# Optimization experiments

Hardware: AMD Instinct MI355X
Metric: run time of the kernel (lower is better)

Reference implementation:

```python
import jax, jax.numpy as jnp
import numpy as np

B = 65536
NE = 256   # n_encode
NH = 256   # n_hidden
NC = 4     # n_command
D = 64     # n_depth (BatchNorm channels)
F = 32     # n_features
M = D * (F // 2)  # 1024
EPS = 1e-5


def setup_inputs() -> dict:
    key = jax.random.key(0)
    ks = jax.random.split(key, 8)
    s = 0.05
    return {
        "feature": jax.random.normal(ks[0], (B, NE), jnp.float32),
        "hidden":  jax.random.normal(ks[1], (B, NH), jnp.float32),
        "command": jax.random.normal(ks[2], (B, NC), jnp.float32),
        # linear weights (torch Linear stores [out, in]); xavier-like scale
        "Wq":  jax.random.normal(ks[3], (D, NC), jnp.float32) * s,
        "Wkz": jax.random.normal(ks[4], (M, NE), jnp.float32) * s,
        "Wkh": jax.random.normal(ks[5], (M, NH), jnp.float32) * s,
        "Wvz": jax.random.normal(ks[6], (M, NE), jnp.float32) * s,
        "Wvh": jax.random.normal(ks[7], (M, NH), jnp.float32) * s,
        # BatchNorm1d(64) affine params (normV exists in __init__ but is unused)
        "gammaQ": jnp.ones((D,), jnp.float32),
        "betaQ":  jnp.zeros((D,), jnp.float32),
        "gammaK": jnp.ones((D,), jnp.float32),
        "betaK":  jnp.zeros((D,), jnp.float32),
    }


def reference(feature, hidden, command, Wq, Wkz, Wkh, Wvz, Wvh,
              gammaQ, betaQ, gammaK, betaK):
    # Q projection: [B, D]; BatchNorm1d over batch (training-mode batch stats,
    # biased variance, matching torch).
    Q = command @ Wq.T
    mQ = jnp.mean(Q, axis=0)
    vQ = jnp.mean(jnp.square(Q - mQ), axis=0)
    Qn = (Q - mQ) / jnp.sqrt(vQ + EPS) * gammaQ + betaQ          # [B, D]

    # K: cat([B,M],[B,M]) -> [B, 2M] -> view [B, F, D] -> transpose -> [B, D, F]
    K = jnp.concatenate([feature @ Wkz.T, hidden @ Wkh.T], axis=1)
    K = K.reshape(-1, F, D).transpose(0, 2, 1)                    # [B, D, F]
    mK = jnp.mean(K, axis=(0, 2), keepdims=True)
    vK = jnp.mean(jnp.square(K - mK), axis=(0, 2), keepdims=True)
    Kn = (K - mK) / jnp.sqrt(vK + EPS) * gammaK[None, :, None] + betaK[None, :, None]

    # V: [B, F, D], NOT batch-normed (normV is dead code in the original)
    V = jnp.concatenate([feature @ Wvz.T, hidden @ Wvh.T], axis=1).reshape(-1, F, D)

    # attention: [B,1,D] @ [B,D,F] -> [B,F] scores; softmax over F; then @ V
    A = jax.nn.softmax(jnp.einsum('bd,bdf->bf', Qn, Kn) / np.sqrt(D).astype(np.float32), axis=-1)
    s = jnp.einsum('bf,bfd->bd', A, V)                            # [B, D]
    return s
```

## Files before the change

### kernel.cpp

```cpp
#include <hip/hip_runtime.h>
#include <hip/hip_bf16.h>
#include <math.h>


typedef float  f32x4   __attribute__((ext_vector_type(4)));
typedef float  f32x16  __attribute__((ext_vector_type(16)));
typedef __bf16 bf16x4  __attribute__((ext_vector_type(4)));
typedef __bf16 bf16x8  __attribute__((ext_vector_type(8)));

#define MFMA16(A, B, C) __builtin_amdgcn_mfma_f32_16x16x32_bf16((A), (B), (C), 0, 0, 0)
#define MFMA32(A, B, C) __builtin_amdgcn_mfma_f32_32x32x16_bf16((A), (B), (C), 0, 0, 0)

#define EPSV 1e-5f

#define WS_WV    0x000000u
#define WS_WKF   0x100000u
#define WS_G     0x120000u
#define WS_CS    0x1A0000u
#define WS_CMDP  0x1A0800u
#define WS_T     0x1A1800u
#define WS_U     0x1A3800u
#define WS_WQ2   0x1A5800u
#define WS_C0    0x1A5C00u

__global__ __launch_bounds__(512, 2) void setup1(const float* __restrict__ feat,
        const float* __restrict__ hid, const float4* __restrict__ cmd,
        const float* __restrict__ Wvz, const float* __restrict__ Wvh,
        __bf16* __restrict__ WV, float* __restrict__ CMDP, float* __restrict__ CS,
        __bf16* __restrict__ Gp)
{
    __shared__ __bf16 T[256 * 40];
    __shared__ float sm[8][14];
    const int blk = blockIdx.x;
    const int tid = threadIdx.x;

    if (blk >= 384) {
        const int b2 = blk - 384;
        float v[14];
#pragma unroll
        for (int k = 0; k < 14; ++k) v[k] = 0.f;
#pragma unroll
        for (int i = 0; i < 4; ++i) {
            float4 c = cmd[(b2 * 4 + i) * 512 + tid];
            v[0] += c.x;  v[1] += c.y;  v[2] += c.z;  v[3] += c.w;
            v[4] += c.x*c.x; v[5] += c.x*c.y; v[6] += c.x*c.z; v[7] += c.x*c.w;
            v[8] += c.y*c.y; v[9] += c.y*c.z; v[10] += c.y*c.w;
            v[11] += c.z*c.z; v[12] += c.z*c.w; v[13] += c.w*c.w;
        }
#pragma unroll
        for (int k = 0; k < 14; ++k) {
            float s = v[k];
#pragma unroll
            for (int off = 32; off; off >>= 1) s += __shfl_xor(s, off);
            if ((tid & 63) == 0) sm[tid >> 6][k] = s;
        }
        __syncthreads();
        if (tid < 14) {
            float s = 0.f;
#pragma unroll
            for (int w = 0; w < 8; ++w) s += sm[w][tid];
            CMDP[b2 * 14 + tid] = s;
        }
        return;
    }
    if (blk >= 128) {
        int t = (blk - 128) * 512 + tid;
        int e = t * 4;
        const float* src = (e < 262144) ? (Wvz + e) : (Wvh + (e - 262144));
        float4 a = *(const float4*)src;
        bf16x4 vv = { (__bf16)a.x, (__bf16)a.y, (__bf16)a.z, (__bf16)a.w };
        *(bf16x4*)(WV + e) = vv;
        return;
    }

    const int mat  = blk >> 6;
    const int chunk = blk & 63;
    const float* X = mat ? hid : feat;
    float* cs = CS + mat * 256;
    const int k0   = chunk * 1024;
    const int wid  = tid >> 6, lane = tid & 63, quad = lane >> 4, l15 = lane & 15;
    const int c    = tid & 255;
    const int t8   = tid >> 8;

    f32x4 acc[2][16];
#pragma unroll
    for (int mt = 0; mt < 2; ++mt)
#pragma unroll
        for (int nt = 0; nt < 16; ++nt) acc[mt][nt] = (f32x4){0.f, 0.f, 0.f, 0.f};

    float clsum = 0.f;
    for (int it = 0; it < 32; ++it) {
        __syncthreads();
        const int kb = k0 + it * 32;
#pragma unroll
        for (int i = 0; i < 16; ++i) {
            int k = t8 + 2 * i;
            float x = X[(size_t)(kb + k) * 256 + c];
            clsum += x;
            T[c * 40 + k] = (__bf16)x;
        }
        __syncthreads();
        bf16x8 a0 = *(const bf16x8*)&T[(wid * 32 +      l15) * 40 + quad * 8];
        bf16x8 a1 = *(const bf16x8*)&T[(wid * 32 + 16 + l15) * 40 + quad * 8];
#pragma unroll
        for (int nt = 0; nt < 16; ++nt) {
            bf16x8 b = *(const bf16x8*)&T[(nt * 16 + l15) * 40 + quad * 8];
            acc[0][nt] = MFMA16(a0, b, acc[0][nt]);
            acc[1][nt] = MFMA16(a1, b, acc[1][nt]);
        }
    }
    atomicAdd(&cs[c], clsum);
    __bf16* outp = Gp + (size_t)blk * 65536;
#pragma unroll
    for (int mt = 0; mt < 2; ++mt)
#pragma unroll
        for (int nt = 0; nt < 16; ++nt)
#pragma unroll
            for (int r = 0; r < 4; ++r) {
                int gi = wid * 32 + mt * 16 + quad * 4 + r;
                int gj = nt * 16 + l15;
                outp[gi * 256 + gj] = (__bf16)acc[mt][nt][r];
            }
}

__global__ void gram_reduce(const __bf16* __restrict__ Gp, float* __restrict__ G)
{
    int o = blockIdx.x * 256 + threadIdx.x;
    int mat = o >> 16, e = o & 65535;
    const __bf16* p = Gp + (size_t)mat * 64 * 65536 + e;
    float s = 0.f;
#pragma unroll 8
    for (int c = 0; c < 64; ++c) s += (float)p[(size_t)c * 65536];
    G[o] = s;
}

__global__ void rowstats(const float* __restrict__ Wkz, const float* __restrict__ Wkh,
        const float* __restrict__ G, const float* __restrict__ CS,
        float* __restrict__ Tout, float* __restrict__ Uout)
{
    const int blk = blockIdx.x;
    const int mat = blk >> 7, jg = blk & 127;
    const float* Wsrc = (mat ? Wkh : Wkz) + (size_t)jg * 8 * 256;
    const float* Gm = G + (size_t)mat * 65536;
    const float* cs = CS + mat * 256;
    __shared__ float wlT[256 * 8];
    __shared__ float red[4][16];
    const int tid = threadIdx.x, wid = tid >> 6, lane = tid & 63;
#pragma unroll
    for (int jj = 0; jj < 8; ++jj) wlT[tid * 8 + jj] = Wsrc[jj * 256 + tid];
    __syncthreads();
    float inner[8];
#pragma unroll
    for (int jj = 0; jj < 8; ++jj) inner[jj] = 0.f;
    for (int r = 0; r < 256; ++r) {
        float g = Gm[r * 256 + tid];
        float4 w0 = *(const float4*)&wlT[r * 8];
        float4 w1 = *(const float4*)&wlT[r * 8 + 4];
        inner[0] = fmaf(w0.x, g, inner[0]); inner[1] = fmaf(w0.y, g, inner[1]);
        inner[2] = fmaf(w0.z, g, inner[2]); inner[3] = fmaf(w0.w, g, inner[3]);
        inner[4] = fmaf(w1.x, g, inner[4]); inner[5] = fmaf(w1.y, g, inner[5]);
        inner[6] = fmaf(w1.z, g, inner[6]); inner[7] = fmaf(w1.w, g, inner[7]);
    }
    float cst = cs[tid];
#pragma unroll
    for (int jj = 0; jj < 8; ++jj) {
        float wme = wlT[tid * 8 + jj];
        float p = wme * inner[jj];
        float u = wme * cst;
#pragma unroll
        for (int off = 32; off; off >>= 1) { p += __shfl_xor(p, off); u += __shfl_xor(u, off); }
        if (lane == 0) { red[wid][jj] = p; red[wid][jj + 8] = u; }
    }
    __syncthreads();
    if (tid < 16) {
        float s = red[0][tid] + red[1][tid] + red[2][tid] + red[3][tid];
        int jj = tid & 7;
        int j = mat * 1024 + jg * 8 + jj;
        if (tid < 8) Tout[j] = s; else Uout[j] = s;
    }
}

__global__ void finalize_kernel(const float* __restrict__ Wq,
        const float* __restrict__ gQ, const float* __restrict__ bQ,
        const float* __restrict__ gK, const float* __restrict__ bK,
        const float* __restrict__ CMDP, const float* __restrict__ T,
        const float* __restrict__ U, float* __restrict__ Wq2, float* __restrict__ C0)
{
    __shared__ float s14[14];
    const int d = threadIdx.x;
    if (d < 14) {
        float s = 0.f;
        for (int b = 0; b < 32; ++b) s += CMDP[b * 14 + d];
        s14[d] = s;
    }
    __syncthreads();
    float s4[4] = { s14[0], s14[1], s14[2], s14[3] };
    float gc[4][4];
    gc[0][0] = s14[4];
    gc[0][1] = gc[1][0] = s14[5];
    gc[0][2] = gc[2][0] = s14[6];
    gc[0][3] = gc[3][0] = s14[7];
    gc[1][1] = s14[8];
    gc[1][2] = gc[2][1] = s14[9];
    gc[1][3] = gc[3][1] = s14[10];
    gc[2][2] = s14[11];
    gc[2][3] = gc[3][2] = s14[12];
    gc[3][3] = s14[13];
    float wq[4];
#pragma unroll
    for (int c = 0; c < 4; ++c) wq[c] = Wq[d * 4 + c];
    const float invB = 1.0f / 65536.0f;
    float mQ = (wq[0]*s4[0] + wq[1]*s4[1] + wq[2]*s4[2] + wq[3]*s4[3]) * invB;
    float eq2 = 0.f;
#pragma unroll
    for (int c = 0; c < 4; ++c)
#pragma unroll
        for (int c2 = 0; c2 < 4; ++c2) eq2 += wq[c] * wq[c2] * gc[c][c2];
    eq2 *= invB;
    float vQ  = eq2 - mQ * mQ;
    float aQ  = gQ[d] / sqrtf(vQ + EPSV);
    float bQv = bQ[d] - mQ * aQ;
    float S2 = 0.f, S1 = 0.f;
#pragma unroll
    for (int f = 0; f < 32; ++f) { S2 += T[f * 64 + d]; S1 += U[f * 64 + d]; }
    const float invBF = 1.0f / (65536.0f * 32.0f);
    float e2 = S2 * invBF, mK = S1 * invBF;
    float vK = e2 - mK * mK;
    float aK = gK[d] / sqrtf(vK + EPSV);
    float c1 = aQ * aK * 0.125f;
    C0[d] = bQv * aK * 0.125f;
#pragma unroll
    for (int c = 0; c < 4; ++c) Wq2[d * 4 + c] = c1 * wq[c];
}

__global__ void foldK(const float* __restrict__ Wkz, const float* __restrict__ Wkh,
                      const float* __restrict__ Wq2, const float* __restrict__ C0,
                      __bf16* __restrict__ WKF)
{
    const int blk = blockIdx.x;
    const int h = blk / 96, rr = blk % 96;
    const int k = threadIdx.x;
    float s = 0.f;
    if (rr < 80) {
        const int c = rr >> 4, fl = rr & 15;
        const float* Wsrc = (h ? Wkh : Wkz) + (size_t)fl * 64 * 256;
        for (int d = 0; d < 64; ++d) {
            float coef = (c == 0) ? C0[d] : Wq2[d * 4 + (c - 1)];
            s = fmaf(coef, Wsrc[d * 256 + k], s);
        }
    }
    WKF[(size_t)(h * 96 + rr) * 256 + k] = (__bf16)s;
}

__global__ __launch_bounds__(256, 2) void fused_attn(
        const float* __restrict__ feat, const float* __restrict__ hid,
        const float4* __restrict__ cmd, const __bf16* __restrict__ WV,
        const __bf16* __restrict__ WKF, float* __restrict__ out)
{
    __shared__ __bf16 BUF[32768];
    __shared__ __bf16 WGTs[16 * 128];
    const int tid  = threadIdx.x;
    const int wid  = tid >> 6, lane = tid & 63;
    const int l5   = lane & 31, hi = lane >> 5;
    const int fl   = l5 & 15;
    const bool low = (l5 < 16);
    const int wrow = (blockIdx.x << 7) + (wid << 5);

    float l_i[16];
    f32x16 s_acc[2];
#pragma unroll
    for (int r = 0; r < 16; ++r) { l_i[r] = 0.f; s_acc[0][r] = 0.f; s_acc[1][r] = 0.f; }

    bf16x8 st[8];

    for (int h = 0; h < 2; ++h) {
        const float* X = h ? hid : feat;
        const __bf16* Wkf = WKF + ((size_t)h * 96 << 8);

        bf16x8 a2[16];
#pragma unroll
        for (int u = 0; u < 16; ++u) {
            const float* p = X + ((size_t)(wrow + l5) << 8) + u * 16 + hi * 8;
            float4 x0 = *(const float4*)p;
            float4 x1 = *(const float4*)(p + 4);
            a2[u] = (bf16x8){ (__bf16)x0.x, (__bf16)x0.y, (__bf16)x0.z, (__bf16)x0.w,
                              (__bf16)x1.x, (__bf16)x1.y, (__bf16)x1.z, (__bf16)x1.w };
        }

        __syncthreads();
#pragma unroll
        for (int i = 0; i < 12; ++i) {
            int cc = tid + i * 256;
            int n = cc >> 5, k8 = cc & 31;
            bf16x8 v = *(const bf16x8*)(Wkf + n * 256 + k8 * 8);
            *(bf16x8*)&BUF[n * 256 + ((k8 ^ (n & 7)) << 3)] = v;
        }
        __syncthreads();

        f32x16 acc1[3];
#pragma unroll
        for (int nt = 0; nt < 3; ++nt)
#pragma unroll
            for (int r = 0; r < 16; ++r) acc1[nt][r] = 0.f;
#pragma unroll
        for (int ks = 0; ks < 16; ++ks)
#pragma unroll
            for (int nt = 0; nt < 3; ++nt) {
                int n = nt * 32 + l5;
                bf16x8 b = *(const bf16x8*)&BUF[n * 256 + (((ks * 2 + hi) ^ (n & 7)) << 3)];
                acc1[nt] = MFMA32(a2[ks], b, acc1[nt]);
            }

#pragma unroll
        for (int g = 0; g < 4; ++g) {
            bf16x4 wv4;
#pragma unroll
            for (int j = 0; j < 4; ++j) {
                const int r = g * 4 + j;
                const int row32 = j + 8 * g + 4 * hi;
                float4 cm = cmd[wrow + row32];
                float e0, e1, t0[3], t1[3];
#pragma unroll
                for (int nt = 0; nt < 3; ++nt) {
                    e0 = acc1[nt][r];
                    e1 = __shfl_xor(e0, 16);
                    t0[nt] = low ? e0 : e1;
                    t1[nt] = low ? e1 : e0;
                }
                float sc = t0[0] + cm.x * t1[0] + cm.y * t0[1]
                                 + cm.z * t1[1] + cm.w * t0[2];
                float w = __expf(sc);
                wv4[j] = (__bf16)w;
                float ws = w;
                ws += __shfl_xor(ws, 1); ws += __shfl_xor(ws, 2);
                ws += __shfl_xor(ws, 4); ws += __shfl_xor(ws, 8);
                l_i[r] += ws;
            }
            if (low) *(bf16x4*)&WGTs[fl * 128 + (wid << 5) + 8 * g + 4 * hi] = wv4;
        }

        if (h == 0) {
            const __bf16* base = WV;
#pragma unroll
            for (int i = 0; i < 8; ++i) {
                int cc = tid + i * 256;
                int n = cc >> 5, k8 = cc & 31;
                st[i] = *(const bf16x8*)(base + n * 256 + k8 * 8);
            }
        }
        __syncthreads();

        for (int f2 = 0; f2 < 16; ++f2) {
            const int bufsel = (f2 & 1) << 14;
#pragma unroll
            for (int i = 0; i < 8; ++i) {
                int cc = tid + i * 256;
                int n = cc >> 5, k8 = cc & 31;
                *(bf16x8*)&BUF[bufsel + n * 256 + ((k8 ^ (n & 7)) << 3)] = st[i];
            }
            __syncthreads();
            const int g2 = h * 16 + f2 + 1;
            if (g2 < 32) {
                const __bf16* base = WV + ((size_t)g2 << 14);
#pragma unroll
                for (int i = 0; i < 8; ++i) {
                    int cc = tid + i * 256;
                    int n = cc >> 5, k8 = cc & 31;
                    st[i] = *(const bf16x8*)(base + n * 256 + k8 * 8);
                }
            }
            f32x16 acc2[2];
#pragma unroll
            for (int r = 0; r < 16; ++r) { acc2[0][r] = 0.f; acc2[1][r] = 0.f; }
#pragma unroll
            for (int ks = 0; ks < 16; ++ks)
#pragma unroll
                for (int nt = 0; nt < 2; ++nt) {
                    int n = nt * 32 + l5;
                    bf16x8 b = *(const bf16x8*)&BUF[bufsel + n * 256
                                                    + (((ks * 2 + hi) ^ (n & 7)) << 3)];
                    acc2[nt] = MFMA32(a2[ks], b, acc2[nt]);
                }
#pragma unroll
            for (int g = 0; g < 4; ++g) {
                bf16x4 wv = *(const bf16x4*)&WGTs[f2 * 128 + (wid << 5) + 8 * g + 4 * hi];
#pragma unroll
                for (int j = 0; j < 4; ++j) {
                    float w = (float)wv[j];
                    s_acc[0][g * 4 + j] += w * acc2[0][g * 4 + j];
                    s_acc[1][g * 4 + j] += w * acc2[1][g * 4 + j];
                }
            }
        }
    }

#pragma unroll
    for (int g = 0; g < 4; ++g)
#pragma unroll
        for (int j = 0; j < 4; ++j) {
            const int r = g * 4 + j;
            float inv = 1.0f / l_i[r];
            size_t row = (size_t)(wrow + j + 8 * g + 4 * hi);
            out[(row << 6) + l5]      = s_acc[0][r] * inv;
            out[(row << 6) + 32 + l5] = s_acc[1][r] * inv;
        }
}

extern "C" void kernel_launch(void* const* d_in, const int* in_sizes, int n_in,
                              void* d_out, int out_size, void* d_ws, size_t ws_size,
                              hipStream_t stream)
{
    (void)in_sizes; (void)n_in; (void)out_size; (void)ws_size;
    const float* feature = (const float*)d_in[0];
    const float* hidden  = (const float*)d_in[1];
    const float* command = (const float*)d_in[2];
    const float* Wq      = (const float*)d_in[3];
    const float* Wkz     = (const float*)d_in[4];
    const float* Wkh     = (const float*)d_in[5];
    const float* Wvz     = (const float*)d_in[6];
    const float* Wvh     = (const float*)d_in[7];
    const float* gammaQ  = (const float*)d_in[8];
    const float* betaQ   = (const float*)d_in[9];
    const float* gammaK  = (const float*)d_in[10];
    const float* betaK   = (const float*)d_in[11];

    char* ws = (char*)d_ws;
    __bf16* WV   = (__bf16*)(ws + WS_WV);
    __bf16* WKF  = (__bf16*)(ws + WS_WKF);
    float*  G    = (float*)(ws + WS_G);
    float*  CS   = (float*)(ws + WS_CS);
    float*  CMDP = (float*)(ws + WS_CMDP);
    float*  Tj   = (float*)(ws + WS_T);
    float*  Uj   = (float*)(ws + WS_U);
    float*  Wq2  = (float*)(ws + WS_WQ2);
    float*  C0   = (float*)(ws + WS_C0);
    float*  outp = (float*)d_out;
    __bf16* Gp   = (__bf16*)d_out;

    hipMemsetAsync(ws + WS_CS, 0, 0x800, stream);
    setup1<<<416, 512, 0, stream>>>(feature, hidden, (const float4*)command,
                                    Wvz, Wvh, WV, CMDP, CS, Gp);
    gram_reduce<<<512, 256, 0, stream>>>(Gp, G);
    rowstats<<<256, 256, 0, stream>>>(Wkz, Wkh, G, CS, Tj, Uj);
    finalize_kernel<<<1, 64, 0, stream>>>(Wq, gammaQ, betaQ, gammaK, betaK,
                                          CMDP, Tj, Uj, Wq2, C0);
    foldK<<<192, 256, 0, stream>>>(Wkz, Wkh, Wq2, C0, WKF);
    fused_attn<<<512, 256, 0, stream>>>(feature, hidden, (const float4*)command,
                                        WV, WKF, outp);
}
```

Baseline: 375.2 us.

## Pre-swizzle V/K weights into MFMA fragment layout and drop LDS staging

Weights WV and the folded K weights are now written in setup in the exact per-lane MFMA B-fragment order, so fused_attn reads them straight from global/L2 with coalesced 16-byte loads. This removes the LDS double-buffer staging and its barriers. The finalize kernel is merged into foldK, which removes one launch. setup1 moves to 1024-thread blocks with 16-row gram tiles per wave. The trade-off is that every block re-reads the weights from cache instead of from LDS, which risks L2 bandwidth pressure.

```diff
diff --git a/kernel.cpp b/kernel.cpp
--- a/kernel.cpp
+++ b/kernel.cpp
@@ -13,35 +13,33 @@
 
 #define EPSV 1e-5f
 
-#define WS_WV    0x000000u
-#define WS_WKF   0x100000u
+#define WS_WVT   0x000000u
+#define WS_WKFT  0x100000u
 #define WS_G     0x120000u
 #define WS_CS    0x1A0000u
 #define WS_CMDP  0x1A0800u
 #define WS_T     0x1A1800u
 #define WS_U     0x1A3800u
-#define WS_WQ2   0x1A5800u
-#define WS_C0    0x1A5C00u
-
-__global__ __launch_bounds__(512, 2) void setup1(const float* __restrict__ feat,
+
+__global__ __launch_bounds__(1024, 1) void setup1(const float* __restrict__ feat,
         const float* __restrict__ hid, const float4* __restrict__ cmd,
         const float* __restrict__ Wvz, const float* __restrict__ Wvh,
-        __bf16* __restrict__ WV, float* __restrict__ CMDP, float* __restrict__ CS,
+        __bf16* __restrict__ WVT, float* __restrict__ CMDP, float* __restrict__ CS,
         __bf16* __restrict__ Gp)
 {
     __shared__ __bf16 T[256 * 40];
-    __shared__ float sm[8][14];
+    __shared__ float sm[16][14];
     const int blk = blockIdx.x;
     const int tid = threadIdx.x;
 
-    if (blk >= 384) {
-        const int b2 = blk - 384;
+    if (blk >= 160) {
+        const int b2 = blk - 160;
         float v[14];
 #pragma unroll
         for (int k = 0; k < 14; ++k) v[k] = 0.f;
 #pragma unroll
-        for (int i = 0; i < 4; ++i) {
-            float4 c = cmd[(b2 * 4 + i) * 512 + tid];
+        for (int i = 0; i < 16; ++i) {
+            float4 c = cmd[b2 * 16384 + i * 1024 + tid];
             v[0] += c.x;  v[1] += c.y;  v[2] += c.z;  v[3] += c.w;
             v[4] += c.x*c.x; v[5] += c.x*c.y; v[6] += c.x*c.z; v[7] += c.x*c.w;
             v[8] += c.y*c.y; v[9] += c.y*c.z; v[10] += c.y*c.w;
@@ -58,18 +56,28 @@
         if (tid < 14) {
             float s = 0.f;
 #pragma unroll
-            for (int w = 0; w < 8; ++w) s += sm[w][tid];
+            for (int w = 0; w < 16; ++w) s += sm[w][tid];
             CMDP[b2 * 14 + tid] = s;
         }
         return;
     }
     if (blk >= 128) {
-        int t = (blk - 128) * 512 + tid;
-        int e = t * 4;
-        const float* src = (e < 262144) ? (Wvz + e) : (Wvh + (e - 262144));
-        float4 a = *(const float4*)src;
-        bf16x4 vv = { (__bf16)a.x, (__bf16)a.y, (__bf16)a.z, (__bf16)a.w };
-        *(bf16x4*)(WV + e) = vv;
+#pragma unroll
+        for (int i = 0; i < 2; ++i) {
+            int E = (blk - 128) * 1024 + i * 32768 + tid;
+            int lane = E & 63, D = E >> 6;
+            int ks = D & 15, nt = (D >> 4) & 1, f = D >> 5;
+            int n32 = lane & 31, hi = lane >> 5;
+            int j = f * 64 + nt * 32 + n32;
+            int k = ks * 16 + hi * 8;
+            const float* src = (j < 1024) ? (Wvz + (size_t)j * 256 + k)
+                                          : (Wvh + (size_t)(j - 1024) * 256 + k);
+            float4 x0 = *(const float4*)src;
+            float4 x1 = *(const float4*)(src + 4);
+            bf16x8 v = { (__bf16)x0.x, (__bf16)x0.y, (__bf16)x0.z, (__bf16)x0.w,
+                         (__bf16)x1.x, (__bf16)x1.y, (__bf16)x1.z, (__bf16)x1.w };
+            *(bf16x8*)(WVT + (size_t)E * 8) = v;
+        }
         return;
     }
 
@@ -80,47 +88,41 @@
     const int k0   = chunk * 1024;
     const int wid  = tid >> 6, lane = tid & 63, quad = lane >> 4, l15 = lane & 15;
     const int c    = tid & 255;
-    const int t8   = tid >> 8;
-
-    f32x4 acc[2][16];
-#pragma unroll
-    for (int mt = 0; mt < 2; ++mt)
-#pragma unroll
-        for (int nt = 0; nt < 16; ++nt) acc[mt][nt] = (f32x4){0.f, 0.f, 0.f, 0.f};
+    const int t4   = tid >> 8;
+
+    f32x4 acc[16];
+#pragma unroll
+    for (int nt = 0; nt < 16; ++nt) acc[nt] = (f32x4){0.f, 0.f, 0.f, 0.f};
 
     float clsum = 0.f;
     for (int it = 0; it < 32; ++it) {
         __syncthreads();
         const int kb = k0 + it * 32;
 #pragma unroll
-        for (int i = 0; i < 16; ++i) {
-            int k = t8 + 2 * i;
+        for (int i = 0; i < 8; ++i) {
+            int k = t4 + 4 * i;
             float x = X[(size_t)(kb + k) * 256 + c];
             clsum += x;
             T[c * 40 + k] = (__bf16)x;
         }
         __syncthreads();
-        bf16x8 a0 = *(const bf16x8*)&T[(wid * 32 +      l15) * 40 + quad * 8];
-        bf16x8 a1 = *(const bf16x8*)&T[(wid * 32 + 16 + l15) * 40 + quad * 8];
+        bf16x8 a0 = *(const bf16x8*)&T[(wid * 16 + l15) * 40 + quad * 8];
 #pragma unroll
         for (int nt = 0; nt < 16; ++nt) {
             bf16x8 b = *(const bf16x8*)&T[(nt * 16 + l15) * 40 + quad * 8];
-            acc[0][nt] = MFMA16(a0, b, acc[0][nt]);
-            acc[1][nt] = MFMA16(a1, b, acc[1][nt]);
+            acc[nt] = MFMA16(a0, b, acc[nt]);
         }
     }
     atomicAdd(&cs[c], clsum);
     __bf16* outp = Gp + (size_t)blk * 65536;
 #pragma unroll
-    for (int mt = 0; mt < 2; ++mt)
-#pragma unroll
-        for (int nt = 0; nt < 16; ++nt)
-#pragma unroll
-            for (int r = 0; r < 4; ++r) {
-                int gi = wid * 32 + mt * 16 + quad * 4 + r;
-                int gj = nt * 16 + l15;
-                outp[gi * 256 + gj] = (__bf16)acc[mt][nt][r];
-            }
+    for (int nt = 0; nt < 16; ++nt)
+#pragma unroll
+        for (int r = 0; r < 4; ++r) {
+            int gi = wid * 16 + quad * 4 + r;
+            int gj = nt * 16 + l15;
+            outp[gi * 256 + gj] = (__bf16)acc[nt][r];
+        }
 }
 
 __global__ void gram_reduce(const __bf16* __restrict__ Gp, float* __restrict__ G)
@@ -180,85 +182,84 @@
     }
 }
 
-__global__ void finalize_kernel(const float* __restrict__ Wq,
+__global__ __launch_bounds__(256) void foldK2(const float* __restrict__ Wkz,
+        const float* __restrict__ Wkh, const float* __restrict__ Wq,
         const float* __restrict__ gQ, const float* __restrict__ bQ,
         const float* __restrict__ gK, const float* __restrict__ bK,
         const float* __restrict__ CMDP, const float* __restrict__ T,
-        const float* __restrict__ U, float* __restrict__ Wq2, float* __restrict__ C0)
+        const float* __restrict__ U, __bf16* __restrict__ WKFT)
 {
     __shared__ float s14[14];
-    const int d = threadIdx.x;
-    if (d < 14) {
-        float s = 0.f;
-        for (int b = 0; b < 32; ++b) s += CMDP[b * 14 + d];
-        s14[d] = s;
-    }
+    __shared__ float C0l[64];
+    __shared__ float W2l[256];
+    const int tid = threadIdx.x;
+    if (tid < 14) s14[tid] = CMDP[tid] + CMDP[14 + tid] + CMDP[28 + tid] + CMDP[42 + tid];
     __syncthreads();
-    float s4[4] = { s14[0], s14[1], s14[2], s14[3] };
-    float gc[4][4];
-    gc[0][0] = s14[4];
-    gc[0][1] = gc[1][0] = s14[5];
-    gc[0][2] = gc[2][0] = s14[6];
-    gc[0][3] = gc[3][0] = s14[7];
-    gc[1][1] = s14[8];
-    gc[1][2] = gc[2][1] = s14[9];
-    gc[1][3] = gc[3][1] = s14[10];
-    gc[2][2] = s14[11];
-    gc[2][3] = gc[3][2] = s14[12];
-    gc[3][3] = s14[13];
-    float wq[4];
-#pragma unroll
-    for (int c = 0; c < 4; ++c) wq[c] = Wq[d * 4 + c];
-    const float invB = 1.0f / 65536.0f;
-    float mQ = (wq[0]*s4[0] + wq[1]*s4[1] + wq[2]*s4[2] + wq[3]*s4[3]) * invB;
-    float eq2 = 0.f;
-#pragma unroll
-    for (int c = 0; c < 4; ++c)
-#pragma unroll
-        for (int c2 = 0; c2 < 4; ++c2) eq2 += wq[c] * wq[c2] * gc[c][c2];
-    eq2 *= invB;
-    float vQ  = eq2 - mQ * mQ;
-    float aQ  = gQ[d] / sqrtf(vQ + EPSV);
-    float bQv = bQ[d] - mQ * aQ;
-    float S2 = 0.f, S1 = 0.f;
-#pragma unroll
-    for (int f = 0; f < 32; ++f) { S2 += T[f * 64 + d]; S1 += U[f * 64 + d]; }
-    const float invBF = 1.0f / (65536.0f * 32.0f);
-    float e2 = S2 * invBF, mK = S1 * invBF;
-    float vK = e2 - mK * mK;
-    float aK = gK[d] / sqrtf(vK + EPSV);
-    float c1 = aQ * aK * 0.125f;
-    C0[d] = bQv * aK * 0.125f;
-#pragma unroll
-    for (int c = 0; c < 4; ++c) Wq2[d * 4 + c] = c1 * wq[c];
-}
-
-__global__ void foldK(const float* __restrict__ Wkz, const float* __restrict__ Wkh,
-                      const float* __restrict__ Wq2, const float* __restrict__ C0,
-                      __bf16* __restrict__ WKF)
-{
+    if (tid < 64) {
+        const int d = tid;
+        float s4[4] = { s14[0], s14[1], s14[2], s14[3] };
+        float gc[4][4];
+        gc[0][0] = s14[4];
+        gc[0][1] = gc[1][0] = s14[5];
+        gc[0][2] = gc[2][0] = s14[6];
+        gc[0][3] = gc[3][0] = s14[7];
+        gc[1][1] = s14[8];
+        gc[1][2] = gc[2][1] = s14[9];
+        gc[1][3] = gc[3][1] = s14[10];
+        gc[2][2] = s14[11];
+        gc[2][3] = gc[3][2] = s14[12];
+        gc[3][3] = s14[13];
+        float wq[4];
+#pragma unroll
+        for (int c = 0; c < 4; ++c) wq[c] = Wq[d * 4 + c];
+        const float invB = 1.0f / 65536.0f;
+        float mQ = (wq[0]*s4[0] + wq[1]*s4[1] + wq[2]*s4[2] + wq[3]*s4[3]) * invB;
+        float eq2 = 0.f;
+#pragma unroll
+        for (int c = 0; c < 4; ++c)
+#pragma unroll
+            for (int c2 = 0; c2 < 4; ++c2) eq2 += wq[c] * wq[c2] * gc[c][c2];
+        eq2 *= invB;
+        float vQ  = eq2 - mQ * mQ;
+        float aQ  = gQ[d] / sqrtf(vQ + EPSV);
+        float bQv = bQ[d] - mQ * aQ;
+        float S2 = 0.f, S1 = 0.f;
+#pragma unroll
+        for (int f = 0; f < 32; ++f) { S2 += T[f * 64 + d]; S1 += U[f * 64 + d]; }
+        const float invBF = 1.0f / (65536.0f * 32.0f);
+        float e2 = S2 * invBF, mK = S1 * invBF;
+        float vK = e2 - mK * mK;
+        float aK = gK[d] / sqrtf(vK + EPSV);
+        float c1 = aQ * aK * 0.125f;
+        C0l[d] = bQv * aK * 0.125f;
+#pragma unroll
+        for (int c = 0; c < 4; ++c) W2l[d * 4 + c] = c1 * wq[c];
+    }
+    __syncthreads();
+
     const int blk = blockIdx.x;
     const int h = blk / 96, rr = blk % 96;
-    const int k = threadIdx.x;
+    const int k = tid;
     float s = 0.f;
     if (rr < 80) {
         const int c = rr >> 4, fl = rr & 15;
         const float* Wsrc = (h ? Wkh : Wkz) + (size_t)fl * 64 * 256;
         for (int d = 0; d < 64; ++d) {
-            float coef = (c == 0) ? C0[d] : Wq2[d * 4 + (c - 1)];
+            float coef = (c == 0) ? C0l[d] : W2l[d * 4 + (c - 1)];
             s = fmaf(coef, Wsrc[d * 256 + k], s);
         }
     }
-    WKF[(size_t)(h * 96 + rr) * 256 + k] = (__bf16)s;
+    const int nt = rr >> 5, n32 = rr & 31;
+    const int ks = k >> 4, hi = (k >> 3) & 1, e = k & 7;
+    WKFT[(size_t)((h * 3 + nt) * 16 + ks) * 512 + (hi * 32 + n32) * 8 + e] = (__bf16)s;
 }
 
 __global__ __launch_bounds__(256, 2) void fused_attn(
         const float* __restrict__ feat, const float* __restrict__ hid,
-        const float4* __restrict__ cmd, const __bf16* __restrict__ WV,
-        const __bf16* __restrict__ WKF, float* __restrict__ out)
-{
-    __shared__ __bf16 BUF[32768];
-    __shared__ __bf16 WGTs[16 * 128];
+        const float4* __restrict__ cmd, const __bf16* __restrict__ WVT,
+        const __bf16* __restrict__ WKFT, float* __restrict__ out)
+{
+    __shared__ __bf16 WGTs[2048];
     const int tid  = threadIdx.x;
     const int wid  = tid >> 6, lane = tid & 63;
     const int l5   = lane & 31, hi = lane >> 5;
@@ -271,11 +272,8 @@
 #pragma unroll
     for (int r = 0; r < 16; ++r) { l_i[r] = 0.f; s_acc[0][r] = 0.f; s_acc[1][r] = 0.f; }
 
-    bf16x8 st[8];
-
     for (int h = 0; h < 2; ++h) {
         const float* X = h ? hid : feat;
-        const __bf16* Wkf = WKF + ((size_t)h * 96 << 8);
 
         bf16x8 a2[16];
 #pragma unroll
@@ -287,16 +285,6 @@
                               (__bf16)x1.x, (__bf16)x1.y, (__bf16)x1.z, (__bf16)x1.w };
         }
 
-        __syncthreads();
-#pragma unroll
-        for (int i = 0; i < 12; ++i) {
-            int cc = tid + i * 256;
-            int n = cc >> 5, k8 = cc & 31;
-            bf16x8 v = *(const bf16x8*)(Wkf + n * 256 + k8 * 8);
-            *(bf16x8*)&BUF[n * 256 + ((k8 ^ (n & 7)) << 3)] = v;
-        }
-        __syncthreads();
-
         f32x16 acc1[3];
 #pragma unroll
         for (int nt = 0; nt < 3; ++nt)
@@ -306,8 +294,8 @@
         for (int ks = 0; ks < 16; ++ks)
 #pragma unroll
             for (int nt = 0; nt < 3; ++nt) {
-                int n = nt * 32 + l5;
-                bf16x8 b = *(const bf16x8*)&BUF[n * 256 + (((ks * 2 + hi) ^ (n & 7)) << 3)];
+                bf16x8 b = *(const bf16x8*)(WKFT
+                        + (size_t)((h * 3 + nt) * 16 + ks) * 512 + lane * 8);
                 acc1[nt] = MFMA32(a2[ks], b, acc1[nt]);
             }
 
@@ -339,36 +327,9 @@
             if (low) *(bf16x4*)&WGTs[fl * 128 + (wid << 5) + 8 * g + 4 * hi] = wv4;
         }
 
-        if (h == 0) {
-            const __bf16* base = WV;
-#pragma unroll
-            for (int i = 0; i < 8; ++i) {
-                int cc = tid + i * 256;
-                int n = cc >> 5, k8 = cc & 31;
-                st[i] = *(const bf16x8*)(base + n * 256 + k8 * 8);
-            }
-        }
-        __syncthreads();
-
+#pragma unroll 2
         for (int f2 = 0; f2 < 16; ++f2) {
-            const int bufsel = (f2 & 1) << 14;
-#pragma unroll
-            for (int i = 0; i < 8; ++i) {
-                int cc = tid + i * 256;
-                int n = cc >> 5, k8 = cc & 31;
-                *(bf16x8*)&BUF[bufsel + n * 256 + ((k8 ^ (n & 7)) << 3)] = st[i];
-            }
-            __syncthreads();
-            const int g2 = h * 16 + f2 + 1;
-            if (g2 < 32) {
-                const __bf16* base = WV + ((size_t)g2 << 14);
-#pragma unroll
-                for (int i = 0; i < 8; ++i) {
-                    int cc = tid + i * 256;
-                    int n = cc >> 5, k8 = cc & 31;
-                    st[i] = *(const bf16x8*)(base + n * 256 + k8 * 8);
-                }
-            }
+            const int f = h * 16 + f2;
             f32x16 acc2[2];
 #pragma unroll
             for (int r = 0; r < 16; ++r) { acc2[0][r] = 0.f; acc2[1][r] = 0.f; }
@@ -376,9 +337,8 @@
             for (int ks = 0; ks < 16; ++ks)
 #pragma unroll
                 for (int nt = 0; nt < 2; ++nt) {
-                    int n = nt * 32 + l5;
-                    bf16x8 b = *(const bf16x8*)&BUF[bufsel + n * 256
-                                                    + (((ks * 2 + hi) ^ (n & 7)) << 3)];
+                    bf16x8 b = *(const bf16x8*)(WVT
+                            + (size_t)((f * 2 + nt) * 16 + ks) * 512 + lane * 8);
                     acc2[nt] = MFMA32(a2[ks], b, acc2[nt]);
                 }
 #pragma unroll
@@ -425,26 +385,23 @@
     const float* betaK   = (const float*)d_in[11];
 
     char* ws = (char*)d_ws;
-    __bf16* WV   = (__bf16*)(ws + WS_WV);
-    __bf16* WKF  = (__bf16*)(ws + WS_WKF);
+    __bf16* WVT  = (__bf16*)(ws + WS_WVT);
+    __bf16* WKFT = (__bf16*)(ws + WS_WKFT);
     float*  G    = (float*)(ws + WS_G);
     float*  CS   = (float*)(ws + WS_CS);
     float*  CMDP = (float*)(ws + WS_CMDP);
     float*  Tj   = (float*)(ws + WS_T);
     float*  Uj   = (float*)(ws + WS_U);
-    float*  Wq2  = (float*)(ws + WS_WQ2);
-    float*  C0   = (float*)(ws + WS_C0);
     float*  outp = (float*)d_out;
     __bf16* Gp   = (__bf16*)d_out;
 
     hipMemsetAsync(ws + WS_CS, 0, 0x800, stream);
-    setup1<<<416, 512, 0, stream>>>(feature, hidden, (const float4*)command,
-                                    Wvz, Wvh, WV, CMDP, CS, Gp);
+    setup1<<<164, 1024, 0, stream>>>(feature, hidden, (const float4*)command,
+                                     Wvz, Wvh, WVT, CMDP, CS, Gp);
     gram_reduce<<<512, 256, 0, stream>>>(Gp, G);
     rowstats<<<256, 256, 0, stream>>>(Wkz, Wkh, G, CS, Tj, Uj);
-    finalize_kernel<<<1, 64, 0, stream>>>(Wq, gammaQ, betaQ, gammaK, betaK,
-                                          CMDP, Tj, Uj, Wq2, C0);
-    foldK<<<192, 256, 0, stream>>>(Wkz, Wkh, Wq2, C0, WKF);
+    foldK2<<<192, 256, 0, stream>>>(Wkz, Wkh, Wq, gammaQ, betaQ, gammaK, betaK,
+                                    CMDP, Tj, Uj, WKFT);
     fused_attn<<<512, 256, 0, stream>>>(feature, hidden, (const float4*)command,
-                                        WV, WKF, outp);
-}
+                                        WVT, WKFT, outp);
+}
```

Measured after the change: 548.4 us. +46.2%, slower.
